# Kernel tuning notes

Hardware: AMD Instinct MI355X
Metric: run time of the kernel (lower is better)

## Reference

```python
import jax, jax.numpy as jnp
import numpy as np


def setup_inputs() -> dict:
    key = jax.random.key(0)
    k1, k2, k3 = jax.random.split(key, 3)
    x = jax.random.normal(k1, (8192, 4096), dtype=jnp.float32)
    # weight initialized in [0,1] per initialize_binary_range (trunc_normal a=0,b=1)
    weight = jax.random.uniform(k2, (4096, 4096), dtype=jnp.float32)
    bias = jax.random.normal(k3, (4096,), dtype=jnp.float32)
    return {"x": x, "weight": weight, "bias": bias}


def binarize_ste(w):
    # forward: clamp(round(w), 0, 1); backward: identity (straight-through)
    w_bin = jnp.clip(jnp.round(w), 0.0, 1.0)
    return w + jax.lax.stop_gradient(w_bin - w)


def reference(x, weight, bias):
    # F.linear(input, W, b) = x @ W.T + b, with binarized weight
    w_b = binarize_ste(weight)
    return jnp.einsum('ni,oi->no', x, w_b) + bias
```

## Files before the change

kernel.cpp:

```cpp
#include <hip/hip_runtime.h>
#include <stdint.h>

typedef __attribute__((ext_vector_type(4))) int int4v;


__device__ __forceinline__ int pack4_rn(float4 v, float s) {
    int a = __float2int_rn(v.x * s) & 0xff;
    int b = __float2int_rn(v.y * s) & 0xff;
    int c = __float2int_rn(v.z * s) & 0xff;
    int d = __float2int_rn(v.w * s) & 0xff;
    return a | (b << 8) | (c << 16) | (d << 24);
}

__device__ __forceinline__ int bin4(float4 v) {
    int a = (v.x > 0.5f) ? 1 : 0;
    int b = (v.y > 0.5f) ? 1 : 0;
    int c = (v.z > 0.5f) ? 1 : 0;
    int d = (v.w > 0.5f) ? 1 : 0;
    return a | (b << 8) | (c << 16) | (d << 24);
}


__global__ __launch_bounds__(256) void lb_quant_x(const float* __restrict__ x,
        signed char* __restrict__ xq, float* __restrict__ rscale, int K)
{
    const int row = blockIdx.x;
    const int tid = threadIdx.x;
    const float* xr = x + (size_t)row * K;

    float mx = 0.f;
    for (int i = tid * 4; i < K; i += 256 * 4) {
        float4 v = *(const float4*)(xr + i);
        mx = fmaxf(mx, fmaxf(fmaxf(fabsf(v.x), fabsf(v.y)),
                             fmaxf(fabsf(v.z), fabsf(v.w))));
    }
#pragma unroll
    for (int s = 32; s; s >>= 1) mx = fmaxf(mx, __shfl_xor(mx, s));
    __shared__ float wmax[4];
    if ((tid & 63) == 0) wmax[tid >> 6] = mx;
    __syncthreads();
    mx = fmaxf(fmaxf(wmax[0], wmax[1]), fmaxf(wmax[2], wmax[3]));

    const float s = (mx > 0.f) ? 127.f / mx : 0.f;
    if (tid == 0) rscale[row] = (mx > 0.f) ? mx * (1.f / 127.f) : 0.f;

    for (int i = tid * 16; i < K; i += 256 * 16) {
        float4 a = *(const float4*)(xr + i);
        float4 b = *(const float4*)(xr + i + 4);
        float4 c = *(const float4*)(xr + i + 8);
        float4 d = *(const float4*)(xr + i + 12);
        int4 o;
        o.x = pack4_rn(a, s); o.y = pack4_rn(b, s);
        o.z = pack4_rn(c, s); o.w = pack4_rn(d, s);
        *(int4*)(xq + (size_t)row * K + i) = o;
    }
}


__global__ void lb_bin_w8(const float* __restrict__ w, int4* __restrict__ wq, long n16) {
    long i = (long)blockIdx.x * blockDim.x + threadIdx.x;
    long stride = (long)gridDim.x * blockDim.x;
    for (; i < n16; i += stride) {
        const float4* p = (const float4*)w + i * 4;
        float4 v0 = p[0], v1 = p[1], v2 = p[2], v3 = p[3];
        int4 o;
        o.x = bin4(v0); o.y = bin4(v1); o.z = bin4(v2); o.w = bin4(v3);
        wq[i] = o;
    }
}


#define BM 256
#define BN 256
#define BK 64
#define TBYTES 16384

#define PHASE_END(T) do { \
    asm volatile("s_waitcnt lgkmcnt(0)" ::: "memory"); \
    __builtin_amdgcn_sched_barrier(0); \
    if ((T) + 3 < nk)           asm volatile("s_waitcnt vmcnt(4)" ::: "memory"); \
    else if ((T) == nk - 3)     asm volatile("s_waitcnt vmcnt(0)" ::: "memory"); \
    __builtin_amdgcn_s_barrier(); \
} while (0)

#define TILE_BODY(CUR, NXT, T) do { \
    if ((T) + 3 < nk) { \
        const int sb_ = ((T) + 3) & 3; \
        stage(Bbase, &ldsB[sb_ * TBYTES], (T) + 3, 0); \
        stage(Bbase, &ldsB[sb_ * TBYTES], (T) + 3, 1); \
        stage(Abase, &ldsA[sb_ * TBYTES], (T) + 3, 0); \
        stage(Abase, &ldsA[sb_ * TBYTES], (T) + 3, 1); \
    } \
    if ((T) + 1 < nk) { \
        const int rb_ = ((T) + 1) & 3; \
        const signed char* ap_ = &ldsA[rb_ * TBYTES + (wr * 128 + fr) * 64]; \
        const signed char* bp_ = &ldsB[rb_ * TBYTES + (wc * 64 + fr) * 64]; \
        _Pragma("unroll") \
        for (int m_ = 0; m_ < 8; ++m_) fA[NXT][m_] = *(const int4v*)(ap_ + m_ * 1024 + sl * 16); \
        _Pragma("unroll") \
        for (int n_ = 0; n_ < 4; ++n_) fB[NXT][n_] = *(const int4v*)(bp_ + n_ * 1024 + sl * 16); \
    } \
    __builtin_amdgcn_s_setprio(1); \
    _Pragma("unroll") \
    for (int m_ = 0; m_ < 8; ++m_) { \
      _Pragma("unroll") \
      for (int n_ = 0; n_ < 4; ++n_) { \
        acc[m_][n_] = __builtin_amdgcn_mfma_i32_16x16x64_i8( \
            fA[CUR][m_], fB[CUR][n_], acc[m_][n_], 0, 0, 0); \
      } \
    } \
    __builtin_amdgcn_s_setprio(0); \
    if ((T) + 1 < nk) PHASE_END(T); \
} while (0)

__global__ __launch_bounds__(512, 2) void lb_gemm256_i8(
    const signed char* __restrict__ A,
    const signed char* __restrict__ B,
    const float* __restrict__ rscale,
    const float* __restrict__ bias,
    float* __restrict__ C,
    int M, int N, int K)
{
    __shared__ signed char ldsA[4 * TBYTES];
    __shared__ signed char ldsB[4 * TBYTES];

    const int tid  = threadIdx.x;
    const int lane = tid & 63;
    const int wave = tid >> 6;
    const int wr   = wave >> 2;
    const int wc   = wave & 3;

    int nwg = gridDim.x;
    int bid = blockIdx.x;
    bid = (bid & 7) * (nwg >> 3) + (bid >> 3);

    const int ntiles = N / BN;
    const int brow = (bid / ntiles) * BM;
    const int bcol = (bid % ntiles) * BN;

    const signed char* Abase = A + (size_t)brow * K;
    const signed char* Bbase = B + (size_t)bcol * K;

    const int srr = tid >> 2;
    const int sg  = tid & 3;
    auto stage = [&](const signed char* gbase, signed char* lbuf, int kt, int c) {
        int rr = c * 128 + srr;
        int gl = (sg - (rr >> 1)) & 3;
        const signed char* src = gbase + (size_t)rr * K + (size_t)kt * BK + gl * 16;
        signed char* dst = lbuf + c * 8192 + tid * 16;
        __builtin_amdgcn_global_load_lds(
            (const __attribute__((address_space(1))) void*)src,
            (__attribute__((address_space(3))) void*)dst, 16, 0, 0);
    };

    const int fr = lane & 15;
    const int fq = lane >> 4;
    const int sl = (fq + (fr >> 1)) & 3;

    int4v acc[8][4];
#pragma unroll
    for (int i = 0; i < 8; ++i)
#pragma unroll
        for (int j = 0; j < 4; ++j)
            acc[i][j] = (int4v){0, 0, 0, 0};

    const int nk = K / BK;

#pragma unroll
    for (int t = 0; t < 3; ++t) {
        stage(Bbase, &ldsB[t * TBYTES], t, 0); stage(Bbase, &ldsB[t * TBYTES], t, 1);
        stage(Abase, &ldsA[t * TBYTES], t, 0); stage(Abase, &ldsA[t * TBYTES], t, 1);
    }
    asm volatile("s_waitcnt vmcnt(4)" ::: "memory");
    __builtin_amdgcn_s_barrier();

    int4v fA[2][8], fB[2][4];
    {
        const signed char* ap_ = &ldsA[(wr * 128 + fr) * 64];
        const signed char* bp_ = &ldsB[(wc * 64 + fr) * 64];
#pragma unroll
        for (int m_ = 0; m_ < 8; ++m_) fA[0][m_] = *(const int4v*)(ap_ + m_ * 1024 + sl * 16);
#pragma unroll
        for (int n_ = 0; n_ < 4; ++n_) fB[0][n_] = *(const int4v*)(bp_ + n_ * 1024 + sl * 16);
    }

    for (int t = 0; t < nk; t += 2) {
        TILE_BODY(0, 1, t);
        TILE_BODY(1, 0, t + 1);
    }

    float bn[4];
#pragma unroll
    for (int n = 0; n < 4; ++n)
        bn[n] = bias[bcol + wc * 64 + n * 16 + fr];

#pragma unroll
    for (int m = 0; m < 8; ++m) {
#pragma unroll
        for (int j = 0; j < 4; ++j) {
            int row = brow + wr * 128 + m * 16 + fq * 4 + j;
            float rs = rscale[row];
#pragma unroll
            for (int n = 0; n < 4; ++n) {
                int col = bcol + wc * 64 + n * 16 + fr;
                C[(size_t)row * N + col] = (float)acc[m][n][j] * rs + bn[n];
            }
        }
    }
}


__global__ __launch_bounds__(256) void lb_gemm_fb(
    const float* __restrict__ x, const float* __restrict__ w,
    const float* __restrict__ bias, float* __restrict__ C,
    int M, int N, int K)
{
    __shared__ float As[16][65];
    __shared__ float Bs[16][65];
    const int tid = threadIdx.x;
    const int tx = tid & 15, ty = tid >> 4;
    const int brow = blockIdx.y * 64, bcol = blockIdx.x * 64;

    float acc[4][4] = {};
    for (int kt = 0; kt < K; kt += 16) {
        for (int i = tid; i < 64 * 16; i += 256) {
            int r = i >> 4, k = i & 15;
            As[k][r] = x[(long)(brow + r) * K + kt + k];
        }
        for (int i = tid; i < 64 * 16; i += 256) {
            int n = i >> 4, k = i & 15;
            Bs[k][n] = (w[(long)(bcol + n) * K + kt + k] > 0.5f) ? 1.f : 0.f;
        }
        __syncthreads();
#pragma unroll
        for (int k = 0; k < 16; ++k) {
            float a[4], b[4];
#pragma unroll
            for (int i = 0; i < 4; ++i) a[i] = As[k][ty * 4 + i];
#pragma unroll
            for (int j = 0; j < 4; ++j) b[j] = Bs[k][tx * 4 + j];
#pragma unroll
            for (int i = 0; i < 4; ++i)
#pragma unroll
                for (int j = 0; j < 4; ++j)
                    acc[i][j] += a[i] * b[j];
        }
        __syncthreads();
    }
#pragma unroll
    for (int i = 0; i < 4; ++i)
#pragma unroll
        for (int j = 0; j < 4; ++j)
            C[(long)(brow + ty * 4 + i) * N + bcol + tx * 4 + j] = acc[i][j] + bias[bcol + tx * 4 + j];
}


extern "C" void kernel_launch(void* const* d_in, const int* in_sizes, int n_in,
                              void* d_out, int out_size, void* d_ws, size_t ws_size,
                              hipStream_t stream) {
    const float* x    = (const float*)d_in[0];
    const float* w    = (const float*)d_in[1];
    const float* bias = (const float*)d_in[2];
    float* out = (float*)d_out;

    const int N = in_sizes[2];
    const int K = in_sizes[1] / N;
    const int M = in_sizes[0] / K;

    const size_t need = (size_t)M * K + (size_t)N * K + (size_t)M * 4;
    const int ngrid = (M / BM) * (N / BN);
    const bool ok = (ws_size >= need) && (M % BM == 0) && (N % BN == 0)
                    && (K % (2 * BK) == 0) && (K / BK >= 4) && (ngrid % 8 == 0);

    if (ok) {
        signed char* xq = (signed char*)d_ws;
        signed char* wq = xq + (size_t)M * K;
        float* rscale   = (float*)(wq + (size_t)N * K);

        lb_quant_x<<<M, 256, 0, stream>>>(x, xq, rscale, K);
        long nw16 = (long)N * K / 16;
        lb_bin_w8<<<2048, 256, 0, stream>>>(w, (int4*)wq, nw16);

        lb_gemm256_i8<<<dim3(ngrid), 512, 0, stream>>>(xq, wq, rscale, bias, out, M, N, K);
    } else {
        dim3 grid(N / 64, M / 64);
        lb_gemm_fb<<<grid, 256, 0, stream>>>(x, w, bias, out, M, N, K);
    }
}
```

Baseline: 227.0 us.

## Replace LDS-staged int8 GEMM with direct global-to-register fragment loads

Removes the LDS staging buffers, global_load_lds pipeline and barriers, and has each wave load its MFMA fragments straight from global memory into registers, double-buffered across two k-steps. The block tile shrinks from 256x256 with 8 waves to 256x128 with 4 waves, so more blocks launch. The aim is to drop LDS traffic and synchronisation overhead, at the cost of no operand sharing between waves and far more global/L2 traffic, which also exposes load latency.

New measurement: 554.7 us. 2.44x slower.

```diff
diff --git a/kernel.cpp b/kernel.cpp
--- a/kernel.cpp
+++ b/kernel.cpp
@@ -71,49 +71,32 @@
 
 
 #define BM 256
-#define BN 256
+#define BN 128
 #define BK 64
-#define TBYTES 16384
-
-#define PHASE_END(T) do { \
-    asm volatile("s_waitcnt lgkmcnt(0)" ::: "memory"); \
-    __builtin_amdgcn_sched_barrier(0); \
-    if ((T) + 3 < nk)           asm volatile("s_waitcnt vmcnt(4)" ::: "memory"); \
-    else if ((T) == nk - 3)     asm volatile("s_waitcnt vmcnt(0)" ::: "memory"); \
-    __builtin_amdgcn_s_barrier(); \
+
+#define LOADF(AF, BF, T) do { \
+    _Pragma("unroll") \
+    for (int m_ = 0; m_ < 8; ++m_) \
+        AF[m_] = *(const int4v*)(Ab + (size_t)m_ * 16 * K + (size_t)(T) * BK); \
+    _Pragma("unroll") \
+    for (int n_ = 0; n_ < 4; ++n_) \
+        BF[n_] = *(const int4v*)(Bb + (size_t)n_ * 16 * K + (size_t)(T) * BK); \
 } while (0)
 
-#define TILE_BODY(CUR, NXT, T) do { \
-    if ((T) + 3 < nk) { \
-        const int sb_ = ((T) + 3) & 3; \
-        stage(Bbase, &ldsB[sb_ * TBYTES], (T) + 3, 0); \
-        stage(Bbase, &ldsB[sb_ * TBYTES], (T) + 3, 1); \
-        stage(Abase, &ldsA[sb_ * TBYTES], (T) + 3, 0); \
-        stage(Abase, &ldsA[sb_ * TBYTES], (T) + 3, 1); \
-    } \
-    if ((T) + 1 < nk) { \
-        const int rb_ = ((T) + 1) & 3; \
-        const signed char* ap_ = &ldsA[rb_ * TBYTES + (wr * 128 + fr) * 64]; \
-        const signed char* bp_ = &ldsB[rb_ * TBYTES + (wc * 64 + fr) * 64]; \
-        _Pragma("unroll") \
-        for (int m_ = 0; m_ < 8; ++m_) fA[NXT][m_] = *(const int4v*)(ap_ + m_ * 1024 + sl * 16); \
-        _Pragma("unroll") \
-        for (int n_ = 0; n_ < 4; ++n_) fB[NXT][n_] = *(const int4v*)(bp_ + n_ * 1024 + sl * 16); \
-    } \
+#define MFMA32(AF, BF) do { \
     __builtin_amdgcn_s_setprio(1); \
     _Pragma("unroll") \
     for (int m_ = 0; m_ < 8; ++m_) { \
       _Pragma("unroll") \
       for (int n_ = 0; n_ < 4; ++n_) { \
         acc[m_][n_] = __builtin_amdgcn_mfma_i32_16x16x64_i8( \
-            fA[CUR][m_], fB[CUR][n_], acc[m_][n_], 0, 0, 0); \
+            AF[m_], BF[n_], acc[m_][n_], 0, 0, 0); \
       } \
     } \
     __builtin_amdgcn_s_setprio(0); \
-    if ((T) + 1 < nk) PHASE_END(T); \
 } while (0)
 
-__global__ __launch_bounds__(512, 2) void lb_gemm256_i8(
+__global__ __launch_bounds__(256, 2) void lb_gemm_i8_direct(
     const signed char* __restrict__ A,
     const signed char* __restrict__ B,
     const float* __restrict__ rscale,
@@ -121,14 +104,11 @@
     float* __restrict__ C,
     int M, int N, int K)
 {
-    __shared__ signed char ldsA[4 * TBYTES];
-    __shared__ signed char ldsB[4 * TBYTES];
-
     const int tid  = threadIdx.x;
     const int lane = tid & 63;
     const int wave = tid >> 6;
-    const int wr   = wave >> 2;
-    const int wc   = wave & 3;
+    const int wr   = wave >> 1;
+    const int wc   = wave & 1;
 
     int nwg = gridDim.x;
     int bid = blockIdx.x;
@@ -138,24 +118,11 @@
     const int brow = (bid / ntiles) * BM;
     const int bcol = (bid % ntiles) * BN;
 
-    const signed char* Abase = A + (size_t)brow * K;
-    const signed char* Bbase = B + (size_t)bcol * K;
-
-    const int srr = tid >> 2;
-    const int sg  = tid & 3;
-    auto stage = [&](const signed char* gbase, signed char* lbuf, int kt, int c) {
-        int rr = c * 128 + srr;
-        int gl = (sg - (rr >> 1)) & 3;
-        const signed char* src = gbase + (size_t)rr * K + (size_t)kt * BK + gl * 16;
-        signed char* dst = lbuf + c * 8192 + tid * 16;
-        __builtin_amdgcn_global_load_lds(
-            (const __attribute__((address_space(1))) void*)src,
-            (__attribute__((address_space(3))) void*)dst, 16, 0, 0);
-    };
-
     const int fr = lane & 15;
     const int fq = lane >> 4;
-    const int sl = (fq + (fr >> 1)) & 3;
+
+    const signed char* Ab = A + (size_t)(brow + wr * 128 + fr) * K + fq * 16;
+    const signed char* Bb = B + (size_t)(bcol + wc * 64 + fr) * K + fq * 16;
 
     int4v acc[8][4];
 #pragma unroll
@@ -166,27 +133,15 @@
 
     const int nk = K / BK;
 
-#pragma unroll
-    for (int t = 0; t < 3; ++t) {
-        stage(Bbase, &ldsB[t * TBYTES], t, 0); stage(Bbase, &ldsB[t * TBYTES], t, 1);
-        stage(Abase, &ldsA[t * TBYTES], t, 0); stage(Abase, &ldsA[t * TBYTES], t, 1);
-    }
-    asm volatile("s_waitcnt vmcnt(4)" ::: "memory");
-    __builtin_amdgcn_s_barrier();
-
-    int4v fA[2][8], fB[2][4];
-    {
-        const signed char* ap_ = &ldsA[(wr * 128 + fr) * 64];
-        const signed char* bp_ = &ldsB[(wc * 64 + fr) * 64];
-#pragma unroll
-        for (int m_ = 0; m_ < 8; ++m_) fA[0][m_] = *(const int4v*)(ap_ + m_ * 1024 + sl * 16);
-#pragma unroll
-        for (int n_ = 0; n_ < 4; ++n_) fB[0][n_] = *(const int4v*)(bp_ + n_ * 1024 + sl * 16);
-    }
+    int4v aF0[8], bF0[4], aF1[8], bF1[4];
+    LOADF(aF0, bF0, 0);
+    LOADF(aF1, bF1, 1);
 
     for (int t = 0; t < nk; t += 2) {
-        TILE_BODY(0, 1, t);
-        TILE_BODY(1, 0, t + 1);
+        MFMA32(aF0, bF0);
+        if (t + 2 < nk) LOADF(aF0, bF0, t + 2);
+        MFMA32(aF1, bF1);
+        if (t + 3 < nk) LOADF(aF1, bF1, t + 3);
     }
 
     float bn[4];
@@ -281,7 +236,7 @@
         long nw16 = (long)N * K / 16;
         lb_bin_w8<<<2048, 256, 0, stream>>>(w, (int4*)wq, nw16);
 
-        lb_gemm256_i8<<<dim3(ngrid), 512, 0, stream>>>(xq, wq, rscale, bias, out, M, N, K);
+        lb_gemm_i8_direct<<<dim3(ngrid), 256, 0, stream>>>(xq, wq, rscale, bias, out, M, N, K);
     } else {
         dim3 grid(N / 64, M / 64);
         lb_gemm_fb<<<grid, 256, 0, stream>>>(x, w, bias, out, M, N, K);
```
